# Optimization experiments

Hardware: AMD Instinct MI355X
Metric: run time of the kernel (lower is better)

Reference implementation:

```python
import jax, jax.numpy as jnp
import numpy as np

T, B, D, H, O = 512, 256, 512, 256, 256
MLP_DIMS = [(D, 100), (100, 100), (100, 100), (100, 50), (50, H)]


def _linear_init(key, fan_in, fan_out):
    kw, kb = jax.random.split(key)
    lim = 1.0 / np.sqrt(fan_in)
    w = jax.random.uniform(kw, (fan_out, fan_in), minval=-lim, maxval=lim, dtype=jnp.float32)
    b = jax.random.uniform(kb, (fan_out,), minval=-lim, maxval=lim, dtype=jnp.float32)
    return w, b


def setup_inputs() -> dict:
    key = jax.random.key(0)
    ks = jax.random.split(key, 8)
    inp = {"x": jax.random.normal(ks[0], (T, B, D), dtype=jnp.float32)}
    for i, (fi, fo) in enumerate(MLP_DIMS):
        w, b = _linear_init(ks[1 + i], fi, fo)
        inp[f"wm{i + 1}"] = w
        inp[f"bm{i + 1}"] = b
    inp["wx"], inp["bx"] = _linear_init(ks[6], D, H)
    inp["wo"], inp["bo"] = _linear_init(ks[7], H, O)
    return inp


def reference(x, wm1, bm1, wm2, bm2, wm3, bm3, wm4, bm4, wm5, bm5, wx, bx, wo, bo):
    def step(h, xt):
        # xt: [B, D], h: [B, H]
        lx = xt @ wx.T + bx                      # linearX
        a = jax.nn.relu(xt @ wm1.T + bm1)        # layerMLP chain
        a = jax.nn.relu(a @ wm2.T + bm2)
        a = jax.nn.relu(a @ wm3.T + bm3)
        a = jax.nn.relu(a @ wm4.T + bm4)
        fx = jax.nn.sigmoid(a @ wm5.T + bm5)
        gate = fx * jax.nn.sigmoid(lx)
        h_new = jax.nn.relu(jnp.roll(h, 1, axis=-1) + gate)
        return h_new, None

    h0 = jnp.zeros((x.shape[1], wx.shape[0]), dtype=x.dtype)
    hidden, _ = jax.lax.scan(step, h0, x)
    output = hidden @ wo.T + bo                  # h2o
    return output, hidden
```

## Files before the change

### kernel.cpp

```cpp
#include <hip/hip_runtime.h>

typedef __attribute__((ext_vector_type(8))) short short8;
typedef __attribute__((ext_vector_type(4))) float f32x4;

#define OFF_WX 0
#define OFF_W1 131072
#define OFF_W2 196608
#define OFF_W3 212992
#define OFF_W4 229376
#define OFF_W5 237568
#define W_TOTAL 253952
#define TR 32

static __device__ __forceinline__ unsigned short f2bf(float f) {
    unsigned int u = __builtin_bit_cast(unsigned int, f);
    unsigned int r = (u + 0x7fffu + ((u >> 16) & 1u)) >> 16;
    return (unsigned short)r;
}
static __device__ __forceinline__ float bf2f(unsigned short h) {
    unsigned int u = ((unsigned int)h) << 16;
    return __builtin_bit_cast(float, u);
}
static __device__ __forceinline__ float sigf(float z) {
    return __builtin_amdgcn_rcpf(1.f + __expf(-z));
}
static __device__ __forceinline__ void stA(unsigned short* dst, int r, int c, float v) {
    dst[(r << 7) + (((c >> 3) ^ (r & 15)) << 3) + (c & 7)] = f2bf(v);
}
static __device__ __forceinline__ int idxG(int r, int c) {
    return (r << 8) + (((c >> 3) ^ (r & 15)) << 3) + (c & 7);
}

#define MFMA(a, bfr, acc) __builtin_amdgcn_mfma_f32_16x16x32_bf16((a), (bfr), (acc), 0, 0, 0)

__global__ __launch_bounds__(256) void prep_kernel(
    const float* __restrict__ wx, const float* __restrict__ wm1,
    const float* __restrict__ wm2, const float* __restrict__ wm3,
    const float* __restrict__ wm4, const float* __restrict__ wm5,
    unsigned short* __restrict__ wb, float* __restrict__ hid)
{
    const int stride = gridDim.x * blockDim.x;
    for (int idx = blockIdx.x * blockDim.x + threadIdx.x; idx < W_TOTAL; idx += stride) {
        float v;
        if (idx < OFF_W1) {
            v = wx[idx];
        } else if (idx < OFF_W2) {
            int j = idx - OFF_W1; int n = j >> 9, k = j & 511;
            v = (n < 100) ? wm1[n * 512 + k] : 0.f;
        } else if (idx < OFF_W3) {
            int j = idx - OFF_W2; int n = j >> 7, k = j & 127;
            v = (n < 100 && k < 100) ? wm2[n * 100 + k] : 0.f;
        } else if (idx < OFF_W4) {
            int j = idx - OFF_W3; int n = j >> 7, k = j & 127;
            v = (n < 100 && k < 100) ? wm3[n * 100 + k] : 0.f;
        } else if (idx < OFF_W5) {
            int j = idx - OFF_W4; int n = j >> 7, k = j & 127;
            v = (n < 50 && k < 100) ? wm4[n * 100 + k] : 0.f;
        } else {
            int j = idx - OFF_W5; int n = j >> 6, k = j & 63;
            v = (k < 50) ? wm5[n * 50 + k] : 0.f;
        }
        wb[idx] = f2bf(v);
    }
    for (int idx = blockIdx.x * blockDim.x + threadIdx.x; idx < 65536; idx += stride)
        hid[idx] = 0.f;
}

__global__ __launch_bounds__(512, 8) void srnn_main(
    const float* __restrict__ x,
    const float* __restrict__ b1, const float* __restrict__ b2,
    const float* __restrict__ b3, const float* __restrict__ b4,
    const float* __restrict__ b5, const float* __restrict__ bx,
    const unsigned short* __restrict__ wb, float* __restrict__ hid)
{
    __shared__ __align__(16) unsigned short Xs[TR * 512];
    __shared__ __align__(16) unsigned short A1[TR * 128];
    unsigned short* A2  = Xs;
    unsigned short* Lxs = Xs + 4096;

    const int tid  = threadIdx.x;
    const int w    = tid >> 6, lane = tid & 63;
    const int blk  = blockIdx.x;
    const int b    = blk >> 4;
    const int t0   = (blk & 15) << 5;
    const int l15  = lane & 15;
    const int rb   = (lane >> 4) << 2;
    const int kp   = (lane >> 4) << 3;

    {
        const int m0 = tid >> 7;
        const int c4 = tid & 127;
        const float* xbase = x + ((size_t)(t0 + m0) * 256 + b) * 512 + (c4 << 2);
        float4 xr[8];
#pragma unroll
        for (int it = 0; it < 8; it++)
            xr[it] = *(const float4*)(xbase + (size_t)it * 524288);
        const int blk8 = c4 >> 1, halfoff = (c4 & 1) << 2;
#pragma unroll
        for (int it = 0; it < 8; it++) {
            const int m = m0 + 4 * it;
            unsigned int p0 = (unsigned int)f2bf(xr[it].x) | ((unsigned int)f2bf(xr[it].y) << 16);
            unsigned int p1 = (unsigned int)f2bf(xr[it].z) | ((unsigned int)f2bf(xr[it].w) << 16);
            *(uint2*)&Xs[(m << 9) + ((blk8 ^ (m & 15)) << 3) + halfoff] = make_uint2(p0, p1);
        }
    }
    __syncthreads();

    f32x4 am1[2], alx[2][2];
    am1[0] = {0,0,0,0}; am1[1] = {0,0,0,0};
#pragma unroll
    for (int i = 0; i < 2; i++) { alx[i][0] = {0,0,0,0}; alx[i][1] = {0,0,0,0}; }
    {
        const unsigned short* W1r  = wb + OFF_W1 + (w * 16 + l15) * 512 + kp;
        const unsigned short* WXr0 = wb + OFF_WX + (w * 16 + l15) * 512 + kp;
        const unsigned short* WXr1 = wb + OFF_WX + ((w + 8) * 16 + l15) * 512 + kp;
#pragma unroll 4
        for (int k0 = 0; k0 < 512; k0 += 32) {
            const int kb = (k0 >> 3) + (lane >> 4);
            const int xo = (kb ^ l15) << 3;
            short8 af0 = *(const short8*)(Xs + (l15 << 9) + xo);
            short8 af1 = *(const short8*)(Xs + ((16 + l15) << 9) + xo);
            short8 b0  = *(const short8*)(W1r + k0);
            short8 bx0 = *(const short8*)(WXr0 + k0);
            short8 bx1 = *(const short8*)(WXr1 + k0);
            am1[0]    = MFMA(af0, b0,  am1[0]);
            am1[1]    = MFMA(af1, b0,  am1[1]);
            alx[0][0] = MFMA(af0, bx0, alx[0][0]);
            alx[0][1] = MFMA(af1, bx0, alx[0][1]);
            alx[1][0] = MFMA(af0, bx1, alx[1][0]);
            alx[1][1] = MFMA(af1, bx1, alx[1][1]);
        }
        const int c = w * 16 + l15;
        const bool ok = (c < 100);
        const float bb = ok ? b1[c] : 0.f;
#pragma unroll
        for (int mt = 0; mt < 2; mt++)
#pragma unroll
            for (int q = 0; q < 4; q++)
                stA(A1, mt * 16 + rb + q, c, ok ? fmaxf(am1[mt][q] + bb, 0.f) : 0.f);
    }
    __syncthreads();

    {
#pragma unroll
        for (int i = 0; i < 2; i++) {
            const int c = (w + 8 * i) * 16 + l15;
            const float bbx = bx[c];
#pragma unroll
            for (int mt = 0; mt < 2; mt++)
#pragma unroll
                for (int q = 0; q < 4; q++) {
                    const int r = mt * 16 + rb + q;
                    Lxs[idxG(r, c)] = f2bf(sigf(alx[i][mt][q] + bbx));
                }
        }
    }

    auto stage23 = [&](const unsigned short* As, const unsigned short* Wg,
                       const float* __restrict__ bias, unsigned short* Ad) {
        f32x4 acc[2];
        acc[0] = {0,0,0,0}; acc[1] = {0,0,0,0};
        const unsigned short* Wr = Wg + (w * 16 + l15) * 128 + kp;
#pragma unroll
        for (int k0 = 0; k0 < 128; k0 += 32) {
            const int kb = (k0 >> 3) + (lane >> 4);
            const int xo = (kb ^ l15) << 3;
            short8 af0 = *(const short8*)(As + (l15 << 7) + xo);
            short8 af1 = *(const short8*)(As + ((16 + l15) << 7) + xo);
            short8 bf  = *(const short8*)(Wr + k0);
            acc[0] = MFMA(af0, bf, acc[0]);
            acc[1] = MFMA(af1, bf, acc[1]);
        }
        const int c = w * 16 + l15;
        const bool ok = (c < 100);
        const float bb = ok ? bias[c] : 0.f;
#pragma unroll
        for (int mt = 0; mt < 2; mt++)
#pragma unroll
            for (int q = 0; q < 4; q++)
                stA(Ad, mt * 16 + rb + q, c, ok ? fmaxf(acc[mt][q] + bb, 0.f) : 0.f);
    };
    stage23(A1, wb + OFF_W2, b2, A2);
    __syncthreads();
    stage23(A2, wb + OFF_W3, b3, A1);
    __syncthreads();

    {
        const int nt = w >> 1, mtl = w & 1;
        f32x4 acc = {0,0,0,0};
        const unsigned short* Wr = wb + OFF_W4 + (nt * 16 + l15) * 128 + kp;
        const int rbase = mtl * 16 + l15;
        const int rxo = rbase & 15;
#pragma unroll
        for (int k0 = 0; k0 < 128; k0 += 32) {
            const int kb = (k0 >> 3) + (lane >> 4);
            short8 af = *(const short8*)(A1 + (rbase << 7) + ((kb ^ rxo) << 3));
            short8 bf = *(const short8*)(Wr + k0);
            acc = MFMA(af, bf, acc);
        }
        const int c = nt * 16 + l15;
        const bool ok = (c < 50);
        const float bb = ok ? b4[c] : 0.f;
#pragma unroll
        for (int q = 0; q < 4; q++)
            stA(A2, mtl * 16 + rb + q, c, ok ? fmaxf(acc[q] + bb, 0.f) : 0.f);
    }
    __syncthreads();

    {
        f32x4 a5[2][2];
#pragma unroll
        for (int i = 0; i < 2; i++) { a5[i][0] = {0,0,0,0}; a5[i][1] = {0,0,0,0}; }
        const unsigned short* W5r0 = wb + OFF_W5 + (w * 16 + l15) * 64 + kp;
        const unsigned short* W5r1 = wb + OFF_W5 + ((w + 8) * 16 + l15) * 64 + kp;
#pragma unroll
        for (int k0 = 0; k0 < 64; k0 += 32) {
            const int kb = (k0 >> 3) + (lane >> 4);
            const int xo = (kb ^ l15) << 3;
            short8 af0 = *(const short8*)(A2 + (l15 << 7) + xo);
            short8 af1 = *(const short8*)(A2 + ((16 + l15) << 7) + xo);
            short8 bf0 = *(const short8*)(W5r0 + k0);
            short8 bf1 = *(const short8*)(W5r1 + k0);
            a5[0][0] = MFMA(af0, bf0, a5[0][0]);
            a5[0][1] = MFMA(af1, bf0, a5[0][1]);
            a5[1][0] = MFMA(af0, bf1, a5[1][0]);
            a5[1][1] = MFMA(af1, bf1, a5[1][1]);
        }
#pragma unroll
        for (int i = 0; i < 2; i++) {
            const int c = (w + 8 * i) * 16 + l15;
            const float bb5 = b5[c];
#pragma unroll
            for (int mt = 0; mt < 2; mt++)
#pragma unroll
                for (int q = 0; q < 4; q++) {
                    const int r = mt * 16 + rb + q;
                    const int ix = idxG(r, c);
                    const float g = sigf(a5[i][mt][q] + bb5) * bf2f(Lxs[ix]);
                    Lxs[ix] = f2bf(g);
                }
        }
    }
    __syncthreads();

    {
        const int j    = tid & 255;
        const int half = tid >> 8;
        const int base = (j + t0 + 1) & 255;
        float ph = 0.f;
#pragma unroll
        for (int mm = 0; mm < 16; mm++) {
            const int m  = half * 16 + mm;
            const int cm = (base + m) & 255;
            ph += bf2f(Lxs[idxG(m, cm)]);
        }
        atomicAdd(hid + b * 256 + j, ph);
    }
}

__global__ __launch_bounds__(256) void out_kernel(
    const float* __restrict__ hid, const float* __restrict__ wo,
    const float* __restrict__ bo, float* __restrict__ out)
{
    __shared__ __align__(16) float hrow[256];
    const int b = blockIdx.x, o = threadIdx.x;
    float h = hid[b * 256 + o];
    hrow[o] = h;
    out[65536 + b * 256 + o] = h;
    __syncthreads();
    const float4* wrow = (const float4*)(wo + o * 256);
    float s = bo[o];
#pragma unroll 8
    for (int k4 = 0; k4 < 64; k4++) {
        float4 w = wrow[k4];
        float4 hh = *(const float4*)&hrow[k4 * 4];
        s += hh.x * w.x + hh.y * w.y + hh.z * w.z + hh.w * w.w;
    }
    out[b * 256 + o] = s;
}

extern "C" void kernel_launch(void* const* d_in, const int* in_sizes, int n_in,
                              void* d_out, int out_size, void* d_ws, size_t ws_size,
                              hipStream_t stream)
{
    (void)in_sizes; (void)n_in; (void)out_size; (void)ws_size;
    const float* x   = (const float*)d_in[0];
    const float* wm1 = (const float*)d_in[1];
    const float* bm1 = (const float*)d_in[2];
    const float* wm2 = (const float*)d_in[3];
    const float* bm2 = (const float*)d_in[4];
    const float* wm3 = (const float*)d_in[5];
    const float* bm3 = (const float*)d_in[6];
    const float* wm4 = (const float*)d_in[7];
    const float* bm4 = (const float*)d_in[8];
    const float* wm5 = (const float*)d_in[9];
    const float* bm5 = (const float*)d_in[10];
    const float* wx  = (const float*)d_in[11];
    const float* bx  = (const float*)d_in[12];
    const float* wo  = (const float*)d_in[13];
    const float* bo  = (const float*)d_in[14];
    float* out = (float*)d_out;

    unsigned short* wb = (unsigned short*)d_ws;
    float* hid = (float*)((char*)d_ws + (size_t)W_TOTAL * 2);

    prep_kernel<<<512, 256, 0, stream>>>(wx, wm1, wm2, wm3, wm4, wm5, wb, hid);
    srnn_main<<<4096, 512, 0, stream>>>(x, bm1, bm2, bm3, bm4, bm5, bx, wb, hid);
    out_kernel<<<256, 256, 0, stream>>>(hid, wo, bo, out);
}
```

Measured before the change: 603.5 us.

## Split fused RNN kernel into staged passes through workspace buffers

When the workspace is large enough, the single fused srnn_main kernel is replaced by three kernels. pass1 computes the first MLP layer and the sigmoid of linearX and stores both as bf16 in global memory. tail runs the remaining MLP layers in per-wave shared tiles and multiplies the result into the gate buffer. reduce sums the rolled gates over time with atomics. The aim is higher occupancy and simpler kernels, at the cost of roughly 100 MB of extra bf16 global traffic and an extra bf16 rounding of the gate.

```diff
diff --git a/kernel.cpp b/kernel.cpp
--- a/kernel.cpp
+++ b/kernel.cpp
@@ -11,6 +11,11 @@
 #define OFF_W5 237568
 #define W_TOTAL 253952
 #define TR 32
+
+#define PB_HID   524288u
+#define PB_A1    786432u
+#define PB_LX    34340864u
+#define PB_NEED  101449728u
 
 static __device__ __forceinline__ unsigned short f2bf(float f) {
     unsigned int u = __builtin_bit_cast(unsigned int, f);
@@ -66,6 +71,232 @@
         hid[idx] = 0.f;
 }
 
+__global__ __launch_bounds__(256, 4) void pass1_kernel(
+    const float* __restrict__ x, const float* __restrict__ b1,
+    const float* __restrict__ bxv, const unsigned short* __restrict__ wb,
+    unsigned short* __restrict__ A1g, unsigned short* __restrict__ Lxg)
+{
+    __shared__ __align__(16) unsigned short Xs[32 * 512];
+
+    const int tid  = threadIdx.x;
+    const int w    = tid >> 6, lane = tid & 63;
+    const int l15  = lane & 15;
+    const int rb   = (lane >> 4) << 2;
+    const int kp   = (lane >> 4) << 3;
+    const size_t r0 = (size_t)blockIdx.x * 32;
+
+    {
+        const float4* xb = (const float4*)(x + r0 * 512);
+        float4 xr[16];
+#pragma unroll
+        for (int it = 0; it < 16; it++)
+            xr[it] = xb[it * 256 + tid];
+#pragma unroll
+        for (int it = 0; it < 16; it++) {
+            const int e = (it * 256 + tid) << 2;
+            const int m = e >> 9, c = e & 511;
+            unsigned int p0 = (unsigned int)f2bf(xr[it].x) | ((unsigned int)f2bf(xr[it].y) << 16);
+            unsigned int p1 = (unsigned int)f2bf(xr[it].z) | ((unsigned int)f2bf(xr[it].w) << 16);
+            *(uint2*)&Xs[(m << 9) + (((c >> 3) ^ (m & 15)) << 3) + (c & 7)] = make_uint2(p0, p1);
+        }
+    }
+    __syncthreads();
+
+    f32x4 am1[2][2], alx[4][2];
+#pragma unroll
+    for (int i = 0; i < 2; i++) { am1[i][0] = {0,0,0,0}; am1[i][1] = {0,0,0,0}; }
+#pragma unroll
+    for (int i = 0; i < 4; i++) { alx[i][0] = {0,0,0,0}; alx[i][1] = {0,0,0,0}; }
+    {
+        const unsigned short* W1p = wb + OFF_W1 + l15 * 512 + kp;
+        const unsigned short* WXp = wb + OFF_WX + l15 * 512 + kp;
+#pragma unroll 4
+        for (int k0 = 0; k0 < 512; k0 += 32) {
+            const int kb = (k0 >> 3) + (lane >> 4);
+            const int xo = (kb ^ l15) << 3;
+            short8 af0 = *(const short8*)(Xs + (l15 << 9) + xo);
+            short8 af1 = *(const short8*)(Xs + ((16 + l15) << 9) + xo);
+#pragma unroll
+            for (int i = 0; i < 2; i++) {
+                short8 bf = *(const short8*)(W1p + ((w + 4 * i) << 13) + k0);
+                am1[i][0] = MFMA(af0, bf, am1[i][0]);
+                am1[i][1] = MFMA(af1, bf, am1[i][1]);
+            }
+#pragma unroll
+            for (int i = 0; i < 4; i++) {
+                short8 bf = *(const short8*)(WXp + ((w + 4 * i) << 13) + k0);
+                alx[i][0] = MFMA(af0, bf, alx[i][0]);
+                alx[i][1] = MFMA(af1, bf, alx[i][1]);
+            }
+        }
+    }
+#pragma unroll
+    for (int i = 0; i < 2; i++) {
+        const int c = (w + 4 * i) * 16 + l15;
+        const bool ok = (c < 100);
+        const float bb = ok ? b1[c] : 0.f;
+#pragma unroll
+        for (int mt = 0; mt < 2; mt++)
+#pragma unroll
+            for (int q = 0; q < 4; q++) {
+                const int r = mt * 16 + rb + q;
+                A1g[(r0 + r) * 128 + c] = f2bf(ok ? fmaxf(am1[i][mt][q] + bb, 0.f) : 0.f);
+            }
+    }
+#pragma unroll
+    for (int i = 0; i < 4; i++) {
+        const int c = (w + 4 * i) * 16 + l15;
+        const float bb = bxv[c];
+#pragma unroll
+        for (int mt = 0; mt < 2; mt++)
+#pragma unroll
+            for (int q = 0; q < 4; q++) {
+                const int r = mt * 16 + rb + q;
+                Lxg[(r0 + r) * 256 + c] = f2bf(sigf(alx[i][mt][q] + bb));
+            }
+    }
+}
+
+__global__ __launch_bounds__(256, 6) void tail_kernel(
+    const float* __restrict__ b2, const float* __restrict__ b3,
+    const float* __restrict__ b4, const float* __restrict__ b5,
+    const unsigned short* __restrict__ wb,
+    const unsigned short* __restrict__ A1g, unsigned short* __restrict__ Lxg)
+{
+    __shared__ __align__(16) unsigned short Sc[4][16 * 128];
+
+    const int tid  = threadIdx.x;
+    const int w    = tid >> 6, lane = tid & 63;
+    const int l15  = lane & 15;
+    const int rb   = (lane >> 4) << 2;
+    const int kp   = (lane >> 4) << 3;
+    unsigned short* Ws = Sc[w];
+    const size_t gr = (size_t)blockIdx.x * 64 + w * 16;
+
+    {
+        short8 af[4];
+#pragma unroll
+        for (int kk = 0; kk < 4; kk++)
+            af[kk] = *(const short8*)(A1g + (gr + l15) * 128 + kk * 32 + kp);
+        f32x4 acc[8];
+#pragma unroll
+        for (int n = 0; n < 8; n++) acc[n] = {0,0,0,0};
+#pragma unroll
+        for (int kk = 0; kk < 4; kk++)
+#pragma unroll
+            for (int n = 0; n < 8; n++) {
+                short8 bf = *(const short8*)(wb + OFF_W2 + (n * 16 + l15) * 128 + kk * 32 + kp);
+                acc[n] = MFMA(af[kk], bf, acc[n]);
+            }
+#pragma unroll
+        for (int n = 0; n < 8; n++) {
+            const int c = n * 16 + l15;
+            const bool ok = (c < 100);
+            const float bb = ok ? b2[c] : 0.f;
+#pragma unroll
+            for (int q = 0; q < 4; q++)
+                stA(Ws, rb + q, c, ok ? fmaxf(acc[n][q] + bb, 0.f) : 0.f);
+        }
+    }
+    {
+        short8 af[4];
+#pragma unroll
+        for (int kk = 0; kk < 4; kk++)
+            af[kk] = *(const short8*)(Ws + (l15 << 7) + ((((kk << 2) + (lane >> 4)) ^ l15) << 3));
+        f32x4 acc[8];
+#pragma unroll
+        for (int n = 0; n < 8; n++) acc[n] = {0,0,0,0};
+#pragma unroll
+        for (int kk = 0; kk < 4; kk++)
+#pragma unroll
+            for (int n = 0; n < 8; n++) {
+                short8 bf = *(const short8*)(wb + OFF_W3 + (n * 16 + l15) * 128 + kk * 32 + kp);
+                acc[n] = MFMA(af[kk], bf, acc[n]);
+            }
+#pragma unroll
+        for (int n = 0; n < 8; n++) {
+            const int c = n * 16 + l15;
+            const bool ok = (c < 100);
+            const float bb = ok ? b3[c] : 0.f;
+#pragma unroll
+            for (int q = 0; q < 4; q++)
+                stA(Ws, rb + q, c, ok ? fmaxf(acc[n][q] + bb, 0.f) : 0.f);
+        }
+    }
+    {
+        short8 af[4];
+#pragma unroll
+        for (int kk = 0; kk < 4; kk++)
+            af[kk] = *(const short8*)(Ws + (l15 << 7) + ((((kk << 2) + (lane >> 4)) ^ l15) << 3));
+        f32x4 acc[4];
+#pragma unroll
+        for (int n = 0; n < 4; n++) acc[n] = {0,0,0,0};
+#pragma unroll
+        for (int kk = 0; kk < 4; kk++)
+#pragma unroll
+            for (int n = 0; n < 4; n++) {
+                short8 bf = *(const short8*)(wb + OFF_W4 + (n * 16 + l15) * 128 + kk * 32 + kp);
+                acc[n] = MFMA(af[kk], bf, acc[n]);
+            }
+#pragma unroll
+        for (int n = 0; n < 4; n++) {
+            const int c = n * 16 + l15;
+            const bool ok = (c < 50);
+            const float bb = ok ? b4[c] : 0.f;
+#pragma unroll
+            for (int q = 0; q < 4; q++)
+                stA(Ws, rb + q, c, ok ? fmaxf(acc[n][q] + bb, 0.f) : 0.f);
+        }
+    }
+    {
+        short8 af[2];
+#pragma unroll
+        for (int kk = 0; kk < 2; kk++)
+            af[kk] = *(const short8*)(Ws + (l15 << 7) + ((((kk << 2) + (lane >> 4)) ^ l15) << 3));
+#pragma unroll
+        for (int h = 0; h < 2; h++) {
+            f32x4 acc[8];
+#pragma unroll
+            for (int n = 0; n < 8; n++) acc[n] = {0,0,0,0};
+#pragma unroll
+            for (int kk = 0; kk < 2; kk++)
+#pragma unroll
+                for (int n = 0; n < 8; n++) {
+                    const int ng = h * 8 + n;
+                    short8 bf = *(const short8*)(wb + OFF_W5 + (ng * 16 + l15) * 64 + kk * 32 + kp);
+                    acc[n] = MFMA(af[kk], bf, acc[n]);
+                }
+#pragma unroll
+            for (int n = 0; n < 8; n++) {
+                const int c = (h * 8 + n) * 16 + l15;
+                const float bb5 = b5[c];
+#pragma unroll
+                for (int q = 0; q < 4; q++) {
+                    const size_t ga = (gr + rb + q) * 256 + c;
+                    const float g = sigf(acc[n][q] + bb5) * bf2f(Lxg[ga]);
+                    Lxg[ga] = f2bf(g);
+                }
+            }
+        }
+    }
+}
+
+__global__ __launch_bounds__(256) void reduce_kernel(
+    const unsigned short* __restrict__ gate, float* __restrict__ hid)
+{
+    const int b  = blockIdx.x >> 2;
+    const int tq = blockIdx.x & 3;
+    const int j  = threadIdx.x;
+    float s = 0.f;
+#pragma unroll 8
+    for (int it = 0; it < 128; it++) {
+        const int t = tq * 128 + it;
+        const int c = (j + t + 1) & 255;
+        s += bf2f(gate[((size_t)(t << 8) + b) * 256 + c]);
+    }
+    atomicAdd(hid + b * 256 + j, s);
+}
+
 __global__ __launch_bounds__(512, 8) void srnn_main(
     const float* __restrict__ x,
     const float* __restrict__ b1, const float* __restrict__ b2,
@@ -283,7 +514,7 @@
                               void* d_out, int out_size, void* d_ws, size_t ws_size,
                               hipStream_t stream)
 {
-    (void)in_sizes; (void)n_in; (void)out_size; (void)ws_size;
+    (void)in_sizes; (void)n_in; (void)out_size;
     const float* x   = (const float*)d_in[0];
     const float* wm1 = (const float*)d_in[1];
     const float* bm1 = (const float*)d_in[2];
@@ -302,9 +533,20 @@
     float* out = (float*)d_out;
 
     unsigned short* wb = (unsigned short*)d_ws;
-    float* hid = (float*)((char*)d_ws + (size_t)W_TOTAL * 2);
-
-    prep_kernel<<<512, 256, 0, stream>>>(wx, wm1, wm2, wm3, wm4, wm5, wb, hid);
-    srnn_main<<<4096, 512, 0, stream>>>(x, bm1, bm2, bm3, bm4, bm5, bx, wb, hid);
-    out_kernel<<<256, 256, 0, stream>>>(hid, wo, bo, out);
-}
+
+    if (ws_size >= (size_t)PB_NEED) {
+        float*          hid = (float*)((char*)d_ws + PB_HID);
+        unsigned short* A1g = (unsigned short*)((char*)d_ws + PB_A1);
+        unsigned short* Lxg = (unsigned short*)((char*)d_ws + PB_LX);
+        prep_kernel<<<512, 256, 0, stream>>>(wx, wm1, wm2, wm3, wm4, wm5, wb, hid);
+        pass1_kernel<<<4096, 256, 0, stream>>>(x, bm1, bx, wb, A1g, Lxg);
+        tail_kernel<<<2048, 256, 0, stream>>>(bm2, bm3, bm4, bm5, wb, A1g, Lxg);
+        reduce_kernel<<<1024, 256, 0, stream>>>(Lxg, hid);
+        out_kernel<<<256, 256, 0, stream>>>(hid, wo, bo, out);
+    } else {
+        float* hid = (float*)((char*)d_ws + (size_t)W_TOTAL * 2);
+        prep_kernel<<<512, 256, 0, stream>>>(wx, wm1, wm2, wm3, wm4, wm5, wb, hid);
+        srnn_main<<<4096, 512, 0, stream>>>(x, bm1, bm2, bm3, bm4, bm5, bx, wb, hid);
+        out_kernel<<<256, 256, 0, stream>>>(hid, wo, bo, out);
+    }
+}
```

Measured after the change: 748.9 us. +24.1%, slower.
